# Optimization experiments

Hardware: AMD Instinct MI355X
Metric: run time of the kernel (lower is better)

## Reference

```python
import jax, jax.numpy as jnp
from jax import lax
import numpy as np

G = 373  # group count
DN = ('NCHW', 'OIHW', 'NCHW')


def gconv(x, w, b):
    # grouped 3x3 conv, padding=1; w: [C_out, C_in/G, 3, 3]
    y = lax.conv_general_dilated(x, w, (1, 1), ((1, 1), (1, 1)),
                                 feature_group_count=G, dimension_numbers=DN)
    return y + b[None, :, None, None]


def gconvT(x, w, b):
    # grouped ConvTranspose2d(k=2, stride=2) == lhs-dilated conv with flipped,
    # in/out-swapped kernel. w (torch layout): [C_in, C_out/G, 2, 2]
    Cin, CoutG, kH, kW = w.shape
    CinG = Cin // G
    wc = w.reshape(G, CinG, CoutG, kH, kW).transpose(0, 2, 1, 3, 4)
    wc = wc.reshape(G * CoutG, CinG, kH, kW)[:, :, ::-1, ::-1]
    y = lax.conv_general_dilated(x, wc, (1, 1), ((kH - 1, kH - 1), (kW - 1, kW - 1)),
                                 lhs_dilation=(2, 2), feature_group_count=G,
                                 dimension_numbers=DN)
    return y + b[None, :, None, None]


def bn(x, g, b, eps=1e-5):
    # BatchNorm2d in training mode: batch statistics over (N, H, W)
    m = jnp.mean(x, (0, 2, 3), keepdims=True)
    v = jnp.var(x, (0, 2, 3), keepdims=True)
    return (x - m) * lax.rsqrt(v + eps) * g[None, :, None, None] + b[None, :, None, None]


def mpool(x, k):
    return lax.reduce_window(x, -jnp.inf, lax.max, (1, 1, k, k), (1, 1, k, k), 'VALID')


def setup_inputs() -> dict:
    key = jax.random.key(0)
    ks = iter(jax.random.split(key, 40))
    rn = lambda shp, s=0.05: jax.random.normal(next(ks), shp, jnp.float32) * s
    d = {'x': jax.random.uniform(next(ks), (16, 373, 64, 64), jnp.float32)}
    # encoder convs (3x3, groups=373)
    d.update(w1=rn((746, 1, 3, 3)), b1=rn((746,)), g1=jnp.ones(746), be1=jnp.zeros(746))
    d.update(w2=rn((1119, 2, 3, 3)), b2=rn((1119,)), g2=jnp.ones(1119), be2=jnp.zeros(1119))
    d.update(w3=rn((1492, 3, 3, 3)), b3=rn((1492,)), g3=jnp.ones(1492), be3=jnp.zeros(1492))
    # decoder transposed convs (2x2 stride 2, groups=373); torch weight layout [Cin, Cout/G, 2, 2]
    d.update(tw1=rn((1492, 3, 2, 2)), tb1=rn((1119,)), tg1=jnp.ones(1119), tbe1=jnp.zeros(1119))
    d.update(tw2=rn((1119, 2, 2, 2)), tb2=rn((746,)), tg2=jnp.ones(746), tbe2=jnp.zeros(746))
    d.update(tw3=rn((746, 1, 2, 2)), tb3=rn((373,)), tg3=jnp.ones(373), tbe3=jnp.zeros(373))
    # encoder2
    d.update(ew=rn((373, 4, 3, 3)), eb=rn((373,)), eg=jnp.ones(373), ebe=jnp.zeros(373))
    # classifier
    d.update(cw=rn((1, 373)), cb=rn((1,)))
    return d


def reference(x, w1, b1, g1, be1, w2, b2, g2, be2, w3, b3, g3, be3,
              tw1, tb1, tg1, tbe1, tw2, tb2, tg2, tbe2, tw3, tb3, tg3, tbe3,
              ew, eb, eg, ebe, cw, cb):
    # encoder: (conv->BN->ReLU->[dropout]->maxpool2) x3; dropout is identity here
    h = mpool(jax.nn.relu(bn(gconv(x, w1, b1), g1, be1)), 2)    # [B,746,32,32]
    h = mpool(jax.nn.relu(bn(gconv(h, w2, b2), g2, be2)), 2)    # [B,1119,16,16]
    enc = mpool(jax.nn.relu(bn(gconv(h, w3, b3), g3, be3)), 2)  # [B,1492,8,8]
    # decoder
    d = jax.nn.relu(bn(gconvT(enc, tw1, tb1), tg1, tbe1))       # [B,1119,16,16]
    d = jax.nn.relu(bn(gconvT(d, tw2, tb2), tg2, tbe2))         # [B,746,32,32]
    decoded = jax.nn.sigmoid(bn(gconvT(d, tw3, tb3), tg3, tbe3))  # [B,373,64,64]
    # encoder2: conv->BN->ReLU->maxpool8 -> [B,373,1,1]
    e2 = mpool(jax.nn.relu(bn(gconv(enc, ew, eb), eg, ebe)), 8)
    # classifier
    flat = e2.reshape(e2.shape[0], -1)                          # [B,373]
    pred = jax.nn.sigmoid(flat @ cw.T + cb)                     # [B,1]
    return decoded, e2, pred
```

## Files before the change

### kernel.cpp

```cpp
#include <hip/hip_runtime.h>
#include <math.h>


__device__ __forceinline__ void block_stats_atomic(float lsum, float lss,
                                                   double* __restrict__ stats, int co) {
#pragma unroll
  for (int o = 32; o > 0; o >>= 1) {
    lsum += __shfl_down(lsum, o, 64);
    lss  += __shfl_down(lss,  o, 64);
  }
  __shared__ float s1[8], s2[8];
  int wid = threadIdx.x >> 6, lane = threadIdx.x & 63;
  if (lane == 0) { s1[wid] = lsum; s2[wid] = lss; }
  __syncthreads();
  if (threadIdx.x == 0) {
    int nw = (blockDim.x + 63) >> 6;
    double ds = 0.0, dss = 0.0;
    for (int i = 0; i < nw; i++) { ds += (double)s1[i]; dss += (double)s2[i]; }
    atomicAdd(&stats[2 * co],     ds);
    atomicAdd(&stats[2 * co + 1], dss);
  }
}

__device__ __forceinline__ void bn_consts(const double* __restrict__ stats,
                                          const float* __restrict__ g,
                                          const float* __restrict__ b,
                                          double inv_cnt, int c,
                                          float& scale, float& shift) {
  const double m   = stats[2 * c] * inv_cnt;
  const double var = stats[2 * c + 1] * inv_cnt - m * m;
  const double sc  = (double)g[c] / sqrt(var + 1e-5);
  scale = (float)sc;
  shift = (float)((double)b[c] - m * sc);
}

template <int CING, bool NORM, int H>
__global__ void gconv_pool2(const float* __restrict__ in, const float* __restrict__ w,
                            const float* __restrict__ bias,
                            const double* __restrict__ in_stats,
                            const float* __restrict__ in_g, const float* __restrict__ in_b,
                            double in_inv_cnt,
                            float* __restrict__ outp, double* __restrict__ stats,
                            int Cin, int Cout, int CoutG) {
  constexpr int W = H;
  constexpr int logW = (H == 64) ? 6 : (H == 32) ? 5 : 4;
  constexpr int plane = H * W;
  constexpr int SW = W + 4;
  constexpr int TSIZE = (H + 2) * SW;
  constexpr int pplane = plane / 4;
  constexpr int Wp = W / 2;
  constexpr int logWp = logW - 1;

  __shared__ float lds[CING * TSIZE];

  const int bx = blockIdx.x;
  const int co = bx % Cout;
  const int n  = bx / Cout;
  const int g  = co / CoutG;
  const float* inb  = in + ((long)n * Cin + (long)g * CING) * plane;
  float*       outb = outp + (long)bx * pplane;
  const int tid = threadIdx.x;
  const int nthr = blockDim.x;

  float nsc[CING], nsh[CING];
  if (NORM) {
#pragma unroll
    for (int ci = 0; ci < CING; ci++)
      bn_consts(in_stats, in_g, in_b, in_inv_cnt, g * CING + ci, nsc[ci], nsh[ci]);
  }

  float wreg[CING * 9];
  const float* wp = w + (long)co * (CING * 9);
#pragma unroll
  for (int i = 0; i < CING * 9; i++) wreg[i] = wp[i];
  const float bs = bias[co];

  for (int i = tid; i < CING * TSIZE / 2; i += nthr)
    ((float2*)lds)[i] = make_float2(0.f, 0.f);
  __syncthreads();

  for (int i = tid; i < CING * (plane / 4); i += nthr) {
    const int ci = i >> (logW + logW - 2);
    const int r  = i & (plane / 4 - 1);
    const int p  = r << 2;
    const int y  = p >> logW, x = p & (W - 1);
    float4 v = *(const float4*)(inb + (long)ci * plane + p);
    if (NORM) {
      v.x = fmaxf(fmaf(v.x, nsc[ci], nsh[ci]), 0.f);
      v.y = fmaxf(fmaf(v.y, nsc[ci], nsh[ci]), 0.f);
      v.z = fmaxf(fmaf(v.z, nsc[ci], nsh[ci]), 0.f);
      v.w = fmaxf(fmaf(v.w, nsc[ci], nsh[ci]), 0.f);
    }
    float* d = lds + ci * TSIZE + (y + 1) * SW + (x + 1);
    d[0] = v.x; d[1] = v.y; d[2] = v.z; d[3] = v.w;
  }
  __syncthreads();

  float lsum = 0.f, lss = 0.f;
  for (int p = tid; p < pplane; p += nthr) {
    const int y0 = (p >> logWp) << 1, x0 = (p & (Wp - 1)) << 1;
    float acc[2][2] = {{bs, bs}, {bs, bs}};
#pragma unroll
    for (int ci = 0; ci < CING; ci++) {
      const float* base = lds + ci * TSIZE + y0 * SW + x0;
#pragma unroll
      for (int dy = 0; dy < 4; ++dy) {
        const float* row = base + dy * SW;
        float v[4];
        v[0] = row[0]; v[1] = row[1]; v[2] = row[2]; v[3] = row[3];
#pragma unroll
        for (int dx = 0; dx < 4; ++dx) {
#pragma unroll
          for (int a = 0; a < 2; ++a) {
            const int ky = dy - a;
            if (ky >= 0 && ky < 3) {
#pragma unroll
              for (int b = 0; b < 2; ++b) {
                const int kx = dx - b;
                if (kx >= 0 && kx < 3)
                  acc[a][b] = fmaf(v[dx], wreg[ci * 9 + ky * 3 + kx], acc[a][b]);
              }
            }
          }
        }
      }
    }
    const float a00 = acc[0][0], a01 = acc[0][1], a10 = acc[1][0], a11 = acc[1][1];
    lsum += a00 + a01 + a10 + a11;
    lss = fmaf(a00, a00, fmaf(a01, a01, fmaf(a10, a10, fmaf(a11, a11, lss))));
    outb[p] = fmaxf(fmaxf(a00, a01), fmaxf(a10, a11));
  }
  block_stats_atomic(lsum, lss, stats, co);
}

__global__ void gconv_pool8(const float* __restrict__ in, const float* __restrict__ w,
                            const float* __restrict__ bias,
                            const double* __restrict__ in_stats,
                            const float* __restrict__ in_g, const float* __restrict__ in_b,
                            double in_inv_cnt,
                            float* __restrict__ outp, double* __restrict__ stats,
                            int Cin, int Cout) {
  const int plane = 64;
  const int bx = blockIdx.x;
  const int co = bx % Cout;
  const int n  = bx / Cout;
  const int g  = co;
  const float* inb = in + ((long)n * Cin + (long)g * 4) * plane;

  float nsc[4], nsh[4];
#pragma unroll
  for (int ci = 0; ci < 4; ci++)
    bn_consts(in_stats, in_g, in_b, in_inv_cnt, g * 4 + ci, nsc[ci], nsh[ci]);

  float wreg[36];
  const float* wp = w + (long)co * 36;
#pragma unroll
  for (int i = 0; i < 36; i++) wreg[i] = wp[i];

  const int y = threadIdx.x >> 3, x = threadIdx.x & 7;
  float acc = bias[co];
#pragma unroll
  for (int ci = 0; ci < 4; ci++) {
    const float* ip = inb + ci * plane;
#pragma unroll
    for (int ky = 0; ky < 3; ky++) {
      const int iy = y + ky - 1;
      if ((unsigned)iy < 8u) {
#pragma unroll
        for (int kx = 0; kx < 3; kx++) {
          const int ix = x + kx - 1;
          if ((unsigned)ix < 8u) {
            float v = ip[(iy << 3) + ix];
            v = fmaxf(fmaf(v, nsc[ci], nsh[ci]), 0.f);
            acc = fmaf(v, wreg[ci * 9 + ky * 3 + kx], acc);
          }
        }
      }
    }
  }
  float lsum = acc, lss = acc * acc, mx = acc;
#pragma unroll
  for (int o = 32; o > 0; o >>= 1) {
    lsum += __shfl_down(lsum, o, 64);
    lss  += __shfl_down(lss,  o, 64);
    mx    = fmaxf(mx, __shfl_down(mx, o, 64));
  }
  if (threadIdx.x == 0) {
    outp[bx] = mx;
    atomicAdd(&stats[2 * co],     (double)lsum);
    atomicAdd(&stats[2 * co + 1], (double)lss);
  }
}

template <int CING, int PIN, int LOGWIN>
__global__ void gconvT2x2(const float* __restrict__ in, const float* __restrict__ w,
                          const float* __restrict__ bias,
                          const double* __restrict__ in_stats,
                          const float* __restrict__ in_g, const float* __restrict__ in_b,
                          double in_inv_cnt,
                          float* __restrict__ out, double* __restrict__ stats,
                          int Cin, int Cout, int CoutG) {
  constexpr int WIN  = 1 << LOGWIN;
  constexpr int WOUT = WIN * 2;
  constexpr int NQ   = PIN / 4;
  const int bx  = blockIdx.x;
  const int co  = bx % Cout;
  const int n   = bx / Cout;
  const int g   = co / CoutG;
  const int cog = co - g * CoutG;
  const float* inb  = in + ((long)n * Cin + (long)g * CING) * PIN;
  float*       outb = out + (long)bx * (PIN * 4);

  float lsum = 0.f, lss = 0.f;
  const int q = threadIdx.x;
  if (q < NQ) {
    float nsc[CING], nsh[CING];
#pragma unroll
    for (int ci = 0; ci < CING; ci++)
      bn_consts(in_stats, in_g, in_b, in_inv_cnt, g * CING + ci, nsc[ci], nsh[ci]);

    float wreg[CING * 4];
#pragma unroll
    for (int ci = 0; ci < CING; ci++) {
#pragma unroll
      for (int t = 0; t < 4; t++)
        wreg[ci * 4 + t] = w[((long)(g * CING + ci) * CoutG + cog) * 4 + t];
    }
    const float bs = bias[co];

    const int p0  = q << 2;
    const int iy  = p0 >> LOGWIN;
    const int ix0 = p0 & (WIN - 1);

    float4 t0a = {bs, bs, bs, bs}, t0b = {bs, bs, bs, bs};
    float4 t1a = {bs, bs, bs, bs}, t1b = {bs, bs, bs, bs};
#pragma unroll
    for (int ci = 0; ci < CING; ci++) {
      float4 v = *(const float4*)(inb + (long)ci * PIN + p0);
      v.x = fmaxf(fmaf(v.x, nsc[ci], nsh[ci]), 0.f);
      v.y = fmaxf(fmaf(v.y, nsc[ci], nsh[ci]), 0.f);
      v.z = fmaxf(fmaf(v.z, nsc[ci], nsh[ci]), 0.f);
      v.w = fmaxf(fmaf(v.w, nsc[ci], nsh[ci]), 0.f);
      const float w0 = wreg[ci * 4 + 0], w1 = wreg[ci * 4 + 1];
      const float w2 = wreg[ci * 4 + 2], w3 = wreg[ci * 4 + 3];
      t0a.x = fmaf(v.x, w0, t0a.x); t0a.y = fmaf(v.x, w1, t0a.y);
      t0a.z = fmaf(v.y, w0, t0a.z); t0a.w = fmaf(v.y, w1, t0a.w);
      t0b.x = fmaf(v.z, w0, t0b.x); t0b.y = fmaf(v.z, w1, t0b.y);
      t0b.z = fmaf(v.w, w0, t0b.z); t0b.w = fmaf(v.w, w1, t0b.w);
      t1a.x = fmaf(v.x, w2, t1a.x); t1a.y = fmaf(v.x, w3, t1a.y);
      t1a.z = fmaf(v.y, w2, t1a.z); t1a.w = fmaf(v.y, w3, t1a.w);
      t1b.x = fmaf(v.z, w2, t1b.x); t1b.y = fmaf(v.z, w3, t1b.y);
      t1b.z = fmaf(v.w, w2, t1b.z); t1b.w = fmaf(v.w, w3, t1b.w);
    }
    float* r0 = outb + (long)(2 * iy) * WOUT + 2 * ix0;
    float* r1 = r0 + WOUT;
    *(float4*)(r0)     = t0a;
    *(float4*)(r0 + 4) = t0b;
    *(float4*)(r1)     = t1a;
    *(float4*)(r1 + 4) = t1b;

    lsum = (t0a.x + t0a.y + t0a.z + t0a.w) + (t0b.x + t0b.y + t0b.z + t0b.w)
         + (t1a.x + t1a.y + t1a.z + t1a.w) + (t1b.x + t1b.y + t1b.z + t1b.w);
    lss  = fmaf(t0a.x, t0a.x, fmaf(t0a.y, t0a.y, fmaf(t0a.z, t0a.z, fmaf(t0a.w, t0a.w, 0.f))));
    lss  = fmaf(t0b.x, t0b.x, fmaf(t0b.y, t0b.y, fmaf(t0b.z, t0b.z, fmaf(t0b.w, t0b.w, lss))));
    lss  = fmaf(t1a.x, t1a.x, fmaf(t1a.y, t1a.y, fmaf(t1a.z, t1a.z, fmaf(t1a.w, t1a.w, lss))));
    lss  = fmaf(t1b.x, t1b.x, fmaf(t1b.y, t1b.y, fmaf(t1b.z, t1b.z, fmaf(t1b.w, t1b.w, lss))));
  }
  block_stats_atomic(lsum, lss, stats, co);
}

__global__ void bn_sigmoid_inplace(float* __restrict__ buf, const double* __restrict__ stats,
                                   const float* __restrict__ gamma, const float* __restrict__ beta,
                                   int C, int plane4, double inv_cnt) {
  const int bx = blockIdx.x;
  const int c  = bx % C;
  float scale, shift;
  bn_consts(stats, gamma, beta, inv_cnt, c, scale, shift);
  float4* b4 = (float4*)buf + (long)bx * plane4;
  for (int p = threadIdx.x; p < plane4; p += blockDim.x) {
    float4 v = b4[p];
    float4 o;
    o.x = 1.f / (1.f + expf(-fmaf(v.x, scale, shift)));
    o.y = 1.f / (1.f + expf(-fmaf(v.y, scale, shift)));
    o.z = 1.f / (1.f + expf(-fmaf(v.z, scale, shift)));
    o.w = 1.f / (1.f + expf(-fmaf(v.w, scale, shift)));
    b4[p] = o;
  }
}

__global__ void e2_classifier(float* __restrict__ e2buf, const double* __restrict__ stats,
                              const float* __restrict__ g, const float* __restrict__ be,
                              const float* __restrict__ cw, const float* __restrict__ cb,
                              float* __restrict__ pred, double inv_cnt) {
  const int n = blockIdx.x, tid = threadIdx.x;
  float contrib = 0.f;
  if (tid < 373) {
    float scale, shift;
    bn_consts(stats, g, be, inv_cnt, tid, scale, shift);
    const float v = fmaxf(fmaf(e2buf[n * 373 + tid], scale, shift), 0.f);
    e2buf[n * 373 + tid] = v;
    contrib = v * cw[tid];
  }
#pragma unroll
  for (int o = 32; o > 0; o >>= 1) contrib += __shfl_down(contrib, o, 64);
  __shared__ float sbuf[6];
  const int wid = tid >> 6;
  if ((tid & 63) == 0) sbuf[wid] = contrib;
  __syncthreads();
  if (tid == 0) {
    float s = 0.f;
    for (int i = 0; i < 6; i++) s += sbuf[i];
    pred[n] = 1.f / (1.f + expf(-(s + cb[0])));
  }
}

extern "C" void kernel_launch(void* const* d_in, const int* in_sizes, int n_in,
                              void* d_out, int out_size, void* d_ws, size_t ws_size,
                              hipStream_t stream) {
  const float* x   = (const float*)d_in[0];
  const float* w1  = (const float*)d_in[1];
  const float* b1  = (const float*)d_in[2];
  const float* g1  = (const float*)d_in[3];
  const float* be1 = (const float*)d_in[4];
  const float* w2  = (const float*)d_in[5];
  const float* b2  = (const float*)d_in[6];
  const float* g2  = (const float*)d_in[7];
  const float* be2 = (const float*)d_in[8];
  const float* w3  = (const float*)d_in[9];
  const float* b3  = (const float*)d_in[10];
  const float* g3  = (const float*)d_in[11];
  const float* be3 = (const float*)d_in[12];
  const float* tw1 = (const float*)d_in[13];
  const float* tb1 = (const float*)d_in[14];
  const float* tg1 = (const float*)d_in[15];
  const float* tbe1= (const float*)d_in[16];
  const float* tw2 = (const float*)d_in[17];
  const float* tb2 = (const float*)d_in[18];
  const float* tg2 = (const float*)d_in[19];
  const float* tbe2= (const float*)d_in[20];
  const float* tw3 = (const float*)d_in[21];
  const float* tb3 = (const float*)d_in[22];
  const float* tg3 = (const float*)d_in[23];
  const float* tbe3= (const float*)d_in[24];
  const float* ew  = (const float*)d_in[25];
  const float* eb  = (const float*)d_in[26];
  const float* eg  = (const float*)d_in[27];
  const float* ebe = (const float*)d_in[28];
  const float* cw  = (const float*)d_in[29];
  const float* cb  = (const float*)d_in[30];

  float* out = (float*)d_out;
  const long DEC = 24444928;
  float* e2_out   = out + DEC;
  float* pred_out = out + DEC + 5968;

  float*  P1 = (float*)d_ws;
  float*  P2 = P1 + 12222464;
  float*  E  = P1 + 16805888;
  double* S  = (double*)(P1 + 18333696);
  const int SL = 2984;

  hipMemsetAsync(S, 0, 8 * SL * sizeof(double), stream);

  const int N = 16;

  gconv_pool2<1, false, 64><<<N * 746, 256, 0, stream>>>(
      x, w1, b1, nullptr, nullptr, nullptr, 0.0, P1, S + 0 * SL, 373, 746, 2);
  gconv_pool2<2, true, 32><<<N * 1119, 256, 0, stream>>>(
      P1, w2, b2, S + 0 * SL, g1, be1, 1.0 / 65536.0, P2, S + 1 * SL, 746, 1119, 3);
  gconv_pool2<3, true, 16><<<N * 1492, 64, 0, stream>>>(
      P2, w3, b3, S + 1 * SL, g2, be2, 1.0 / 16384.0, E, S + 2 * SL, 1119, 1492, 4);

  gconv_pool8<<<N * 373, 64, 0, stream>>>(
      E, ew, eb, S + 2 * SL, g3, be3, 1.0 / 4096.0, e2_out, S + 6 * SL, 1492, 373);
  e2_classifier<<<N, 384, 0, stream>>>(
      e2_out, S + 6 * SL, eg, ebe, cw, cb, pred_out, 1.0 / 1024.0);

  gconvT2x2<4, 64, 3><<<N * 1119, 64, 0, stream>>>(
      E, tw1, tb1, S + 2 * SL, g3, be3, 1.0 / 4096.0, P2, S + 3 * SL, 1492, 1119, 3);
  gconvT2x2<3, 256, 4><<<N * 746, 64, 0, stream>>>(
      P2, tw2, tb2, S + 3 * SL, tg1, tbe1, 1.0 / 4096.0, P1, S + 4 * SL, 1119, 746, 2);
  gconvT2x2<2, 1024, 5><<<N * 373, 256, 0, stream>>>(
      P1, tw3, tb3, S + 4 * SL, tg2, tbe2, 1.0 / 16384.0, out, S + 5 * SL, 746, 373, 1);
  bn_sigmoid_inplace<<<N * 373, 256, 0, stream>>>(
      out, S + 5 * SL, tg3, tbe3, 373, 1024, 1.0 / 65536.0);
}
```

Measured before the change: 418.2 us.

## Process all output channels of a group per block with 8-wide register strips

Result: faster. 355.7 us (-14.9%).

```diff
diff --git a/kernel.cpp b/kernel.cpp
--- a/kernel.cpp
+++ b/kernel.cpp
@@ -1,26 +1,6 @@
 #include <hip/hip_runtime.h>
 #include <math.h>
 
-
-__device__ __forceinline__ void block_stats_atomic(float lsum, float lss,
-                                                   double* __restrict__ stats, int co) {
-#pragma unroll
-  for (int o = 32; o > 0; o >>= 1) {
-    lsum += __shfl_down(lsum, o, 64);
-    lss  += __shfl_down(lss,  o, 64);
-  }
-  __shared__ float s1[8], s2[8];
-  int wid = threadIdx.x >> 6, lane = threadIdx.x & 63;
-  if (lane == 0) { s1[wid] = lsum; s2[wid] = lss; }
-  __syncthreads();
-  if (threadIdx.x == 0) {
-    int nw = (blockDim.x + 63) >> 6;
-    double ds = 0.0, dss = 0.0;
-    for (int i = 0; i < nw; i++) { ds += (double)s1[i]; dss += (double)s2[i]; }
-    atomicAdd(&stats[2 * co],     ds);
-    atomicAdd(&stats[2 * co + 1], dss);
-  }
-}
 
 __device__ __forceinline__ void bn_consts(const double* __restrict__ stats,
                                           const float* __restrict__ g,
@@ -34,40 +14,99 @@
   shift = (float)((double)b[c] - m * sc);
 }
 
-template <int CING, bool NORM, int H>
-__global__ void gconv_pool2(const float* __restrict__ in, const float* __restrict__ w,
-                            const float* __restrict__ bias,
-                            const double* __restrict__ in_stats,
-                            const float* __restrict__ in_g, const float* __restrict__ in_b,
-                            double in_inv_cnt,
-                            float* __restrict__ outp, double* __restrict__ stats,
-                            int Cin, int Cout, int CoutG) {
-  constexpr int W = H;
-  constexpr int logW = (H == 64) ? 6 : (H == 32) ? 5 : 4;
-  constexpr int plane = H * W;
-  constexpr int SW = W + 4;
-  constexpr int TSIZE = (H + 2) * SW;
-  constexpr int pplane = plane / 4;
-  constexpr int Wp = W / 2;
-  constexpr int logWp = logW - 1;
+template <int SUBG>
+__device__ __forceinline__ void subgroup_stats(float lsum, float lss,
+                                               double* __restrict__ stats, int co) {
+#pragma unroll
+  for (int o = SUBG / 2; o > 0; o >>= 1) {
+    lsum += __shfl_down(lsum, o, SUBG);
+    lss  += __shfl_down(lss,  o, SUBG);
+  }
+  if ((threadIdx.x & (SUBG - 1)) == 0) {
+    atomicAdd(&stats[2 * co],     (double)lsum);
+    atomicAdd(&stats[2 * co + 1], (double)lss);
+  }
+}
+
+template <int CING, int COUTG, int H, bool NORM>
+__global__ __launch_bounds__(COUTG*(H/2)*(H/8)) void gconv_pool2(
+    const float* __restrict__ in, const float* __restrict__ w,
+    const float* __restrict__ bias,
+    const double* __restrict__ in_stats,
+    const float* __restrict__ in_g, const float* __restrict__ in_b,
+    double in_inv_cnt,
+    float* __restrict__ outp, double* __restrict__ stats,
+    int Cin, int Cout) {
+  constexpr int W      = H;
+  constexpr int logW   = (H == 64) ? 6 : (H == 32) ? 5 : 4;
+  constexpr int SW     = W + 8;
+  constexpr int SWC    = SW / 4;
+  constexpr int TSIZE  = (H + 2) * SW;
+  constexpr int TC     = TSIZE / 4;
+  constexpr int PLANE  = H * W;
+  constexpr int PP4    = PLANE / 4;
+  constexpr int STRIPS = (H / 2) * (W / 8);
+  constexpr int SPR    = W / 8;
+  constexpr int THREADS= COUTG * STRIPS;
+  constexpr int PPOOL  = PLANE / 4;
+  constexpr int SUBG   = (STRIPS < 64) ? STRIPS : 64;
 
   __shared__ float lds[CING * TSIZE];
-
-  const int bx = blockIdx.x;
-  const int co = bx % Cout;
-  const int n  = bx / Cout;
-  const int g  = co / CoutG;
-  const float* inb  = in + ((long)n * Cin + (long)g * CING) * plane;
-  float*       outb = outp + (long)bx * pplane;
+  __shared__ float sA[CING], sB[CING];
+
+  const int bx  = blockIdx.x;
+  const int n   = bx / 373;
+  const int g   = bx % 373;
   const int tid = threadIdx.x;
-  const int nthr = blockDim.x;
-
-  float nsc[CING], nsh[CING];
+
+  const float* inb = in + ((long)n * Cin + (long)g * CING) * PLANE;
+
   if (NORM) {
-#pragma unroll
-    for (int ci = 0; ci < CING; ci++)
-      bn_consts(in_stats, in_g, in_b, in_inv_cnt, g * CING + ci, nsc[ci], nsh[ci]);
-  }
+    if (tid < CING) {
+      float sc, sh;
+      bn_consts(in_stats, in_g, in_b, in_inv_cnt, g * CING + tid, sc, sh);
+      sA[tid] = sc; sB[tid] = sh;
+    }
+    __syncthreads();
+  }
+
+  constexpr int PCZ = 2 * SWC + 2 * H;
+  for (int i = tid; i < CING * PCZ; i += THREADS) {
+    const int ci = i / PCZ;
+    const int z  = i - ci * PCZ;
+    int row, cc;
+    if (z < SWC)              { row = 0;                 cc = z; }
+    else if (z < 2 * SWC)     { row = H + 1;             cc = z - SWC; }
+    else if (z < 2 * SWC + H) { row = z - 2 * SWC + 1;   cc = 0; }
+    else                      { row = z - 2 * SWC - H + 1; cc = SWC - 1; }
+    const int c = (row * SWC + cc) ^ ((row >> 1) & 1);
+    ((float4*)lds)[ci * TC + c] = make_float4(0.f, 0.f, 0.f, 0.f);
+  }
+
+  for (int i = tid; i < CING * PP4; i += THREADS) {
+    const int ci = i >> (logW + logW - 2);
+    const int p4 = i & (PP4 - 1);
+    const int y  = p4 >> (logW - 2);
+    const int x  = (p4 << 2) & (W - 1);
+    float4 v = *(const float4*)(inb + (long)ci * PLANE + (p4 << 2));
+    if (NORM) {
+      const float sc = sA[ci], sh = sB[ci];
+      v.x = fmaxf(fmaf(v.x, sc, sh), 0.f);
+      v.y = fmaxf(fmaf(v.y, sc, sh), 0.f);
+      v.z = fmaxf(fmaf(v.z, sc, sh), 0.f);
+      v.w = fmaxf(fmaf(v.w, sc, sh), 0.f);
+    }
+    const int row = y + 1;
+    const int c   = (row * SWC + 1 + (x >> 2)) ^ ((row >> 1) & 1);
+    ((float4*)lds)[ci * TC + c] = v;
+  }
+  __syncthreads();
+
+  const int co_l = tid / STRIPS;
+  const int s    = tid & (STRIPS - 1);
+  const int y0   = (s / SPR) * 2;
+  const int x0   = (s & (SPR - 1)) * 8;
+  const int co   = g * COUTG + co_l;
 
   float wreg[CING * 9];
   const float* wp = w + (long)co * (CING * 9);
@@ -75,62 +114,59 @@
   for (int i = 0; i < CING * 9; i++) wreg[i] = wp[i];
   const float bs = bias[co];
 
-  for (int i = tid; i < CING * TSIZE / 2; i += nthr)
-    ((float2*)lds)[i] = make_float2(0.f, 0.f);
-  __syncthreads();
-
-  for (int i = tid; i < CING * (plane / 4); i += nthr) {
-    const int ci = i >> (logW + logW - 2);
-    const int r  = i & (plane / 4 - 1);
-    const int p  = r << 2;
-    const int y  = p >> logW, x = p & (W - 1);
-    float4 v = *(const float4*)(inb + (long)ci * plane + p);
-    if (NORM) {
-      v.x = fmaxf(fmaf(v.x, nsc[ci], nsh[ci]), 0.f);
-      v.y = fmaxf(fmaf(v.y, nsc[ci], nsh[ci]), 0.f);
-      v.z = fmaxf(fmaf(v.z, nsc[ci], nsh[ci]), 0.f);
-      v.w = fmaxf(fmaf(v.w, nsc[ci], nsh[ci]), 0.f);
-    }
-    float* d = lds + ci * TSIZE + (y + 1) * SW + (x + 1);
-    d[0] = v.x; d[1] = v.y; d[2] = v.z; d[3] = v.w;
-  }
-  __syncthreads();
-
-  float lsum = 0.f, lss = 0.f;
-  for (int p = tid; p < pplane; p += nthr) {
-    const int y0 = (p >> logWp) << 1, x0 = (p & (Wp - 1)) << 1;
-    float acc[2][2] = {{bs, bs}, {bs, bs}};
-#pragma unroll
-    for (int ci = 0; ci < CING; ci++) {
-      const float* base = lds + ci * TSIZE + y0 * SW + x0;
-#pragma unroll
-      for (int dy = 0; dy < 4; ++dy) {
-        const float* row = base + dy * SW;
-        float v[4];
-        v[0] = row[0]; v[1] = row[1]; v[2] = row[2]; v[3] = row[3];
-#pragma unroll
-        for (int dx = 0; dx < 4; ++dx) {
-#pragma unroll
-          for (int a = 0; a < 2; ++a) {
-            const int ky = dy - a;
-            if (ky >= 0 && ky < 3) {
-#pragma unroll
-              for (int b = 0; b < 2; ++b) {
-                const int kx = dx - b;
-                if (kx >= 0 && kx < 3)
-                  acc[a][b] = fmaf(v[dx], wreg[ci * 9 + ky * 3 + kx], acc[a][b]);
-              }
-            }
+  float acc[2][8];
+#pragma unroll
+  for (int a = 0; a < 2; a++)
+#pragma unroll
+    for (int j = 0; j < 8; j++) acc[a][j] = bs;
+
+#pragma unroll
+  for (int ci = 0; ci < CING; ci++) {
+    const float4* pl = (const float4*)lds + ci * TC;
+#pragma unroll
+    for (int dy = 0; dy < 4; dy++) {
+      const int row = y0 + dy;
+      const int cb  = row * SWC + (x0 >> 2);
+      const int sz  = (row >> 1) & 1;
+      float v[16];
+#pragma unroll
+      for (int k = 0; k < 4; k++) {
+        const float4 q = pl[(cb + k) ^ sz];
+        v[4 * k] = q.x; v[4 * k + 1] = q.y; v[4 * k + 2] = q.z; v[4 * k + 3] = q.w;
+      }
+#pragma unroll
+      for (int a = 0; a < 2; a++) {
+        const int ky = dy - a;
+        if (ky >= 0 && ky < 3) {
+#pragma unroll
+          for (int kx = 0; kx < 3; kx++) {
+            const float wv = wreg[ci * 9 + ky * 3 + kx];
+#pragma unroll
+            for (int j = 0; j < 8; j++)
+              acc[a][j] = fmaf(v[j + 3 + kx], wv, acc[a][j]);
           }
         }
       }
     }
-    const float a00 = acc[0][0], a01 = acc[0][1], a10 = acc[1][0], a11 = acc[1][1];
-    lsum += a00 + a01 + a10 + a11;
-    lss = fmaf(a00, a00, fmaf(a01, a01, fmaf(a10, a10, fmaf(a11, a11, lss))));
-    outb[p] = fmaxf(fmaxf(a00, a01), fmaxf(a10, a11));
-  }
-  block_stats_atomic(lsum, lss, stats, co);
+  }
+
+  float lsum = 0.f, lss = 0.f;
+#pragma unroll
+  for (int a = 0; a < 2; a++)
+#pragma unroll
+    for (int j = 0; j < 8; j++) {
+      lsum += acc[a][j];
+      lss   = fmaf(acc[a][j], acc[a][j], lss);
+    }
+  float4 pv;
+  pv.x = fmaxf(fmaxf(acc[0][0], acc[0][1]), fmaxf(acc[1][0], acc[1][1]));
+  pv.y = fmaxf(fmaxf(acc[0][2], acc[0][3]), fmaxf(acc[1][2], acc[1][3]));
+  pv.z = fmaxf(fmaxf(acc[0][4], acc[0][5]), fmaxf(acc[1][4], acc[1][5]));
+  pv.w = fmaxf(fmaxf(acc[0][6], acc[0][7]), fmaxf(acc[1][6], acc[1][7]));
+  float* outb = outp + ((long)n * Cout + co) * PPOOL + (y0 >> 1) * (W / 2) + (x0 >> 1);
+  *(float4*)outb = pv;
+
+  subgroup_stats<SUBG>(lsum, lss, stats, co);
 }
 
 __global__ void gconv_pool8(const float* __restrict__ in, const float* __restrict__ w,
@@ -192,81 +228,87 @@
   }
 }
 
-template <int CING, int PIN, int LOGWIN>
-__global__ void gconvT2x2(const float* __restrict__ in, const float* __restrict__ w,
-                          const float* __restrict__ bias,
-                          const double* __restrict__ in_stats,
-                          const float* __restrict__ in_g, const float* __restrict__ in_b,
-                          double in_inv_cnt,
-                          float* __restrict__ out, double* __restrict__ stats,
-                          int Cin, int Cout, int CoutG) {
-  constexpr int WIN  = 1 << LOGWIN;
-  constexpr int WOUT = WIN * 2;
-  constexpr int NQ   = PIN / 4;
+template <int CING, int COUTG, int PIN, int LOGWIN, int THREADS>
+__global__ __launch_bounds__(THREADS) void gconvT2x2(
+    const float* __restrict__ in, const float* __restrict__ w,
+    const float* __restrict__ bias,
+    const double* __restrict__ in_stats,
+    const float* __restrict__ in_g, const float* __restrict__ in_b,
+    double in_inv_cnt,
+    float* __restrict__ out, double* __restrict__ stats,
+    int Cin, int Cout) {
+  constexpr int WIN    = 1 << LOGWIN;
+  constexpr int WOUT   = WIN * 2;
+  constexpr int NQ     = PIN / 4;
+  constexpr int LOGNQ  = (NQ == 16) ? 4 : (NQ == 64) ? 6 : 8;
+  constexpr int ACTIVE = COUTG * NQ;
+  constexpr int SUBG   = (NQ < 64) ? NQ : 64;
+
   const int bx  = blockIdx.x;
-  const int co  = bx % Cout;
-  const int n   = bx / Cout;
-  const int g   = co / CoutG;
-  const int cog = co - g * CoutG;
+  const int n   = bx / 373;
+  const int g   = bx % 373;
+  const int tid = threadIdx.x;
+  if (tid >= ACTIVE) return;
+  const int co_l = tid >> LOGNQ;
+  const int q    = tid & (NQ - 1);
+  const int co   = g * COUTG + co_l;
   const float* inb  = in + ((long)n * Cin + (long)g * CING) * PIN;
-  float*       outb = out + (long)bx * (PIN * 4);
-
-  float lsum = 0.f, lss = 0.f;
-  const int q = threadIdx.x;
-  if (q < NQ) {
-    float nsc[CING], nsh[CING];
-#pragma unroll
-    for (int ci = 0; ci < CING; ci++)
-      bn_consts(in_stats, in_g, in_b, in_inv_cnt, g * CING + ci, nsc[ci], nsh[ci]);
-
-    float wreg[CING * 4];
-#pragma unroll
-    for (int ci = 0; ci < CING; ci++) {
-#pragma unroll
-      for (int t = 0; t < 4; t++)
-        wreg[ci * 4 + t] = w[((long)(g * CING + ci) * CoutG + cog) * 4 + t];
-    }
-    const float bs = bias[co];
-
-    const int p0  = q << 2;
-    const int iy  = p0 >> LOGWIN;
-    const int ix0 = p0 & (WIN - 1);
-
-    float4 t0a = {bs, bs, bs, bs}, t0b = {bs, bs, bs, bs};
-    float4 t1a = {bs, bs, bs, bs}, t1b = {bs, bs, bs, bs};
-#pragma unroll
-    for (int ci = 0; ci < CING; ci++) {
-      float4 v = *(const float4*)(inb + (long)ci * PIN + p0);
-      v.x = fmaxf(fmaf(v.x, nsc[ci], nsh[ci]), 0.f);
-      v.y = fmaxf(fmaf(v.y, nsc[ci], nsh[ci]), 0.f);
-      v.z = fmaxf(fmaf(v.z, nsc[ci], nsh[ci]), 0.f);
-      v.w = fmaxf(fmaf(v.w, nsc[ci], nsh[ci]), 0.f);
-      const float w0 = wreg[ci * 4 + 0], w1 = wreg[ci * 4 + 1];
-      const float w2 = wreg[ci * 4 + 2], w3 = wreg[ci * 4 + 3];
-      t0a.x = fmaf(v.x, w0, t0a.x); t0a.y = fmaf(v.x, w1, t0a.y);
-      t0a.z = fmaf(v.y, w0, t0a.z); t0a.w = fmaf(v.y, w1, t0a.w);
-      t0b.x = fmaf(v.z, w0, t0b.x); t0b.y = fmaf(v.z, w1, t0b.y);
-      t0b.z = fmaf(v.w, w0, t0b.z); t0b.w = fmaf(v.w, w1, t0b.w);
-      t1a.x = fmaf(v.x, w2, t1a.x); t1a.y = fmaf(v.x, w3, t1a.y);
-      t1a.z = fmaf(v.y, w2, t1a.z); t1a.w = fmaf(v.y, w3, t1a.w);
-      t1b.x = fmaf(v.z, w2, t1b.x); t1b.y = fmaf(v.z, w3, t1b.y);
-      t1b.z = fmaf(v.w, w2, t1b.z); t1b.w = fmaf(v.w, w3, t1b.w);
-    }
-    float* r0 = outb + (long)(2 * iy) * WOUT + 2 * ix0;
-    float* r1 = r0 + WOUT;
-    *(float4*)(r0)     = t0a;
-    *(float4*)(r0 + 4) = t0b;
-    *(float4*)(r1)     = t1a;
-    *(float4*)(r1 + 4) = t1b;
-
-    lsum = (t0a.x + t0a.y + t0a.z + t0a.w) + (t0b.x + t0b.y + t0b.z + t0b.w)
-         + (t1a.x + t1a.y + t1a.z + t1a.w) + (t1b.x + t1b.y + t1b.z + t1b.w);
-    lss  = fmaf(t0a.x, t0a.x, fmaf(t0a.y, t0a.y, fmaf(t0a.z, t0a.z, fmaf(t0a.w, t0a.w, 0.f))));
-    lss  = fmaf(t0b.x, t0b.x, fmaf(t0b.y, t0b.y, fmaf(t0b.z, t0b.z, fmaf(t0b.w, t0b.w, lss))));
-    lss  = fmaf(t1a.x, t1a.x, fmaf(t1a.y, t1a.y, fmaf(t1a.z, t1a.z, fmaf(t1a.w, t1a.w, lss))));
-    lss  = fmaf(t1b.x, t1b.x, fmaf(t1b.y, t1b.y, fmaf(t1b.z, t1b.z, fmaf(t1b.w, t1b.w, lss))));
-  }
-  block_stats_atomic(lsum, lss, stats, co);
+  float*       outb = out + ((long)n * Cout + co) * (PIN * 4);
+
+  float nsc[CING], nsh[CING];
+#pragma unroll
+  for (int ci = 0; ci < CING; ci++)
+    bn_consts(in_stats, in_g, in_b, in_inv_cnt, g * CING + ci, nsc[ci], nsh[ci]);
+
+  float wreg[CING * 4];
+#pragma unroll
+  for (int ci = 0; ci < CING; ci++) {
+#pragma unroll
+    for (int t = 0; t < 4; t++)
+      wreg[ci * 4 + t] = w[((long)(g * CING + ci) * COUTG + co_l) * 4 + t];
+  }
+  const float bs = bias[co];
+
+  const int p0  = q << 2;
+  const int iy  = p0 >> LOGWIN;
+  const int ix0 = p0 & (WIN - 1);
+
+  float4 t0a = {bs, bs, bs, bs}, t0b = {bs, bs, bs, bs};
+  float4 t1a = {bs, bs, bs, bs}, t1b = {bs, bs, bs, bs};
+#pragma unroll
+  for (int ci = 0; ci < CING; ci++) {
+    float4 v = *(const float4*)(inb + (long)ci * PIN + p0);
+    v.x = fmaxf(fmaf(v.x, nsc[ci], nsh[ci]), 0.f);
+    v.y = fmaxf(fmaf(v.y, nsc[ci], nsh[ci]), 0.f);
+    v.z = fmaxf(fmaf(v.z, nsc[ci], nsh[ci]), 0.f);
+    v.w = fmaxf(fmaf(v.w, nsc[ci], nsh[ci]), 0.f);
+    const float w0 = wreg[ci * 4 + 0], w1 = wreg[ci * 4 + 1];
+    const float w2 = wreg[ci * 4 + 2], w3 = wreg[ci * 4 + 3];
+    t0a.x = fmaf(v.x, w0, t0a.x); t0a.y = fmaf(v.x, w1, t0a.y);
+    t0a.z = fmaf(v.y, w0, t0a.z); t0a.w = fmaf(v.y, w1, t0a.w);
+    t0b.x = fmaf(v.z, w0, t0b.x); t0b.y = fmaf(v.z, w1, t0b.y);
+    t0b.z = fmaf(v.w, w0, t0b.z); t0b.w = fmaf(v.w, w1, t0b.w);
+    t1a.x = fmaf(v.x, w2, t1a.x); t1a.y = fmaf(v.x, w3, t1a.y);
+    t1a.z = fmaf(v.y, w2, t1a.z); t1a.w = fmaf(v.y, w3, t1a.w);
+    t1b.x = fmaf(v.z, w2, t1b.x); t1b.y = fmaf(v.z, w3, t1b.y);
+    t1b.z = fmaf(v.w, w2, t1b.z); t1b.w = fmaf(v.w, w3, t1b.w);
+  }
+  float* r0 = outb + (long)(2 * iy) * WOUT + 2 * ix0;
+  float* r1 = r0 + WOUT;
+  *(float4*)(r0)     = t0a;
+  *(float4*)(r0 + 4) = t0b;
+  *(float4*)(r1)     = t1a;
+  *(float4*)(r1 + 4) = t1b;
+
+  float lsum = (t0a.x + t0a.y + t0a.z + t0a.w) + (t0b.x + t0b.y + t0b.z + t0b.w)
+             + (t1a.x + t1a.y + t1a.z + t1a.w) + (t1b.x + t1b.y + t1b.z + t1b.w);
+  float lss;
+  lss = fmaf(t0a.x, t0a.x, fmaf(t0a.y, t0a.y, fmaf(t0a.z, t0a.z, t0a.w * t0a.w)));
+  lss = fmaf(t0b.x, t0b.x, fmaf(t0b.y, t0b.y, fmaf(t0b.z, t0b.z, fmaf(t0b.w, t0b.w, lss))));
+  lss = fmaf(t1a.x, t1a.x, fmaf(t1a.y, t1a.y, fmaf(t1a.z, t1a.z, fmaf(t1a.w, t1a.w, lss))));
+  lss = fmaf(t1b.x, t1b.x, fmaf(t1b.y, t1b.y, fmaf(t1b.z, t1b.z, fmaf(t1b.w, t1b.w, lss))));
+
+  subgroup_stats<SUBG>(lsum, lss, stats, co);
 }
 
 __global__ void bn_sigmoid_inplace(float* __restrict__ buf, const double* __restrict__ stats,
@@ -363,25 +405,26 @@
   hipMemsetAsync(S, 0, 8 * SL * sizeof(double), stream);
 
   const int N = 16;
-
-  gconv_pool2<1, false, 64><<<N * 746, 256, 0, stream>>>(
-      x, w1, b1, nullptr, nullptr, nullptr, 0.0, P1, S + 0 * SL, 373, 746, 2);
-  gconv_pool2<2, true, 32><<<N * 1119, 256, 0, stream>>>(
-      P1, w2, b2, S + 0 * SL, g1, be1, 1.0 / 65536.0, P2, S + 1 * SL, 746, 1119, 3);
-  gconv_pool2<3, true, 16><<<N * 1492, 64, 0, stream>>>(
-      P2, w3, b3, S + 1 * SL, g2, be2, 1.0 / 16384.0, E, S + 2 * SL, 1119, 1492, 4);
+  const int NG = N * 373;
+
+  gconv_pool2<1, 2, 64, false><<<NG, 512, 0, stream>>>(
+      x, w1, b1, nullptr, nullptr, nullptr, 0.0, P1, S + 0 * SL, 373, 746);
+  gconv_pool2<2, 3, 32, true><<<NG, 192, 0, stream>>>(
+      P1, w2, b2, S + 0 * SL, g1, be1, 1.0 / 65536.0, P2, S + 1 * SL, 746, 1119);
+  gconv_pool2<3, 4, 16, true><<<NG, 64, 0, stream>>>(
+      P2, w3, b3, S + 1 * SL, g2, be2, 1.0 / 16384.0, E, S + 2 * SL, 1119, 1492);
 
   gconv_pool8<<<N * 373, 64, 0, stream>>>(
       E, ew, eb, S + 2 * SL, g3, be3, 1.0 / 4096.0, e2_out, S + 6 * SL, 1492, 373);
   e2_classifier<<<N, 384, 0, stream>>>(
       e2_out, S + 6 * SL, eg, ebe, cw, cb, pred_out, 1.0 / 1024.0);
 
-  gconvT2x2<4, 64, 3><<<N * 1119, 64, 0, stream>>>(
-      E, tw1, tb1, S + 2 * SL, g3, be3, 1.0 / 4096.0, P2, S + 3 * SL, 1492, 1119, 3);
-  gconvT2x2<3, 256, 4><<<N * 746, 64, 0, stream>>>(
-      P2, tw2, tb2, S + 3 * SL, tg1, tbe1, 1.0 / 4096.0, P1, S + 4 * SL, 1119, 746, 2);
-  gconvT2x2<2, 1024, 5><<<N * 373, 256, 0, stream>>>(
-      P1, tw3, tb3, S + 4 * SL, tg2, tbe2, 1.0 / 16384.0, out, S + 5 * SL, 746, 373, 1);
+  gconvT2x2<4, 3, 64, 3, 64><<<NG, 64, 0, stream>>>(
+      E, tw1, tb1, S + 2 * SL, g3, be3, 1.0 / 4096.0, P2, S + 3 * SL, 1492, 1119);
+  gconvT2x2<3, 2, 256, 4, 128><<<NG, 128, 0, stream>>>(
+      P2, tw2, tb2, S + 3 * SL, tg1, tbe1, 1.0 / 4096.0, P1, S + 4 * SL, 1119, 746);
+  gconvT2x2<2, 1, 1024, 5, 256><<<NG, 256, 0, stream>>>(
+      P1, tw3, tb3, S + 4 * SL, tg2, tbe2, 1.0 / 16384.0, out, S + 5 * SL, 746, 373);
   bn_sigmoid_inplace<<<N * 373, 256, 0, stream>>>(
       out, S + 5 * SL, tg3, tbe3, 373, 1024, 1.0 / 65536.0);
 }
```
